# Performance work log

Hardware: AMD Instinct MI355X
Metric: run time of the kernel (lower is better)

The kernel has to match this reference:

```python
import jax, jax.numpy as jnp
import numpy as np

N = 50000       # num nodes
E = 800000      # num edges (before self loops)
D_IN = 128
D_H = 128
D_OUT = 40


def setup_inputs() -> dict:
    key = jax.random.key(0)
    ks = jax.random.split(key, 8)
    x = jax.random.normal(ks[0], (N, D_IN), dtype=jnp.float32)
    edge_index = jax.random.randint(ks[1], (2, E), 0, N, dtype=jnp.int32)
    # GCNConv weights (glorot-ish scale) and biases
    W1 = jax.random.normal(ks[2], (D_IN, D_H), dtype=jnp.float32) / np.sqrt(D_IN)
    b1 = jnp.zeros((D_H,), dtype=jnp.float32)
    W2 = jax.random.normal(ks[3], (D_H, D_H), dtype=jnp.float32) / np.sqrt(D_H)
    b2 = jnp.zeros((D_H,), dtype=jnp.float32)
    Wc = jax.random.normal(ks[4], (D_H, D_OUT), dtype=jnp.float32) / np.sqrt(D_H)
    bc = jnp.zeros((D_OUT,), dtype=jnp.float32)
    return {"x": x, "edge_index": edge_index, "W1": W1, "b1": b1,
            "W2": W2, "b2": b2, "Wc": Wc, "bc": bc}


def _gcn_conv(x, row, col, num_nodes, W, b):
    # PyG GCNConv: h = X @ W; out[c] += norm(r,c) * h[r]; out += b
    h = x @ W
    deg = jax.ops.segment_sum(jnp.ones(row.shape[0], h.dtype), col,
                              num_segments=num_nodes)
    dinv = jnp.where(deg > 0, jax.lax.rsqrt(deg), 0.0).astype(h.dtype)
    norm = dinv[row] * dinv[col]                      # [E+N]
    msg = h[row] * norm[:, None]                      # gather + scale
    agg = jax.ops.segment_sum(msg, col, num_segments=num_nodes)  # scatter-add
    return agg + b


def reference(x, edge_index, W1, b1, W2, b2, Wc, bc):
    # add self loops (GCNConv default add_self_loops=True)
    loops = jnp.arange(N, dtype=edge_index.dtype)
    row = jnp.concatenate([edge_index[0], loops])
    col = jnp.concatenate([edge_index[1], loops])
    h = jax.nn.relu(_gcn_conv(x, row, col, N, W1, b1))
    h = jax.nn.relu(_gcn_conv(h, row, col, N, W2, b2))
    g = jnp.mean(h, axis=0)                           # mean pool over nodes
    return g @ Wc + bc                                # [D_OUT]
```

## Files before the change

### kernel.cpp

```cpp
#include <hip/hip_runtime.h>
#include <hip/hip_fp16.h>


typedef _Float16 half8 __attribute__((ext_vector_type(8)));
typedef float f32x4 __attribute__((ext_vector_type(4)));
typedef float f32x2 __attribute__((ext_vector_type(2)));

constexpr int N = 50000;
constexpr int E = 800000;
constexpr int D = 128;
constexpr int DOUT = 40;
constexpr int CAP = 64;
constexpr int HB = 128;
constexpr int EPB = E / HB;
constexpr int HWRD = 12500;
constexpr int GM = (N + 127) / 128;
constexpr int NW = N / 4;
constexpr int GF = 3 * GM;
constexpr int GB2 = (N + 31) / 32;

__global__ __launch_bounds__(1024) void k_hist(const int* __restrict__ col,
                                               unsigned char* __restrict__ hist,
                                               unsigned char* __restrict__ rank,
                                               const float* __restrict__ W1,
                                               const float* __restrict__ W2,
                                               __half* __restrict__ T1,
                                               __half* __restrict__ T2) {
    __shared__ unsigned int h[HWRD];
    int b = blockIdx.x, t = threadIdx.x;
    if (b >= HB) {
        int o = (b - HB) * 1024 + t;
        const float* W = (o < 16384) ? W1 : W2;
        __half* T = (o < 16384) ? T1 : T2;
        int oo = o & 16383;
        int n = oo >> 7, k = oo & 127;
        T[oo] = (__half)W[k * 128 + n];
        return;
    }
    for (int i = t; i < HWRD; i += 1024) h[i] = 0;
    __syncthreads();
    int e0 = b * EPB;
    for (int e = e0 + t; e < e0 + EPB; e += 1024) {
        int c = col[e];
        unsigned int old = atomicAdd(&h[c >> 2], 1u << ((c & 3) * 8));
        rank[e] = (unsigned char)((old >> ((c & 3) * 8)) & 0xff);
    }
    __syncthreads();
    unsigned int* out = (unsigned int*)(hist + (size_t)b * 50000);
    for (int i = t; i < HWRD; i += 1024) out[i] = h[i];
}

__global__ void k_colscan(unsigned char* __restrict__ hist, int* __restrict__ deg,
                          float* __restrict__ dinv) {
    int c4 = blockIdx.x * 256 + threadIdx.x;
    if (c4 >= HWRD) return;
    unsigned int* hw = (unsigned int*)hist;
    unsigned int run = 0;
#pragma unroll 8
    for (int b = 0; b < HB; ++b) {
        unsigned int v = hw[b * HWRD + c4];
        hw[b * HWRD + c4] = run;
        run += v;
    }
#pragma unroll
    for (int j = 0; j < 4; ++j) {
        int dg = (run >> (8 * j)) & 0xff;
        deg[4 * c4 + j] = dg;
        dinv[4 * c4 + j] = rsqrtf((float)(dg + 1));
    }
}

__device__ __forceinline__ unsigned char f8enc(float v) {
    return (unsigned char)(__builtin_amdgcn_cvt_pk_fp8_f32(v, v, 0, false) & 0xff);
}
__device__ __forceinline__ void add8f8(float* a, uint2 u) {
    f32x2 f0 = __builtin_amdgcn_cvt_pk_f32_fp8(u.x, false);
    f32x2 f1 = __builtin_amdgcn_cvt_pk_f32_fp8(u.x, true);
    f32x2 f2 = __builtin_amdgcn_cvt_pk_f32_fp8(u.y, false);
    f32x2 f3 = __builtin_amdgcn_cvt_pk_f32_fp8(u.y, true);
    a[0] += f0[0]; a[1] += f0[1]; a[2] += f1[0]; a[3] += f1[1];
    a[4] += f2[0]; a[5] += f2[1]; a[6] += f3[0]; a[7] += f3[1];
}

__device__ __forceinline__ half8 ldA(const float* rowp, int koff) {
    float4 u0 = *(const float4*)(rowp + koff);
    float4 u1 = *(const float4*)(rowp + koff + 4);
    half8 r;
    r[0] = (_Float16)u0.x; r[1] = (_Float16)u0.y;
    r[2] = (_Float16)u0.z; r[3] = (_Float16)u0.w;
    r[4] = (_Float16)u1.x; r[5] = (_Float16)u1.y;
    r[6] = (_Float16)u1.z; r[7] = (_Float16)u1.w;
    return r;
}

__device__ __forceinline__ void mfma_gemm(const float* __restrict__ A,
                                          const __half* __restrict__ Wt,
                                          const float* __restrict__ dinv,
                                          unsigned char* __restrict__ out8,
                                          int row0, int tid) {
    int wave = tid >> 6, lane = tid & 63;
    int quad = lane >> 4, c16 = lane & 15;
    int m0 = row0 + wave * 32;
    int ra = m0 + c16;      if (ra >= N) ra = 0;
    int rb = m0 + 16 + c16; if (rb >= N) rb = 0;
    const float* pa = A + (size_t)ra * D;
    const float* pb = A + (size_t)rb * D;

    f32x4 acc[2][8];
#pragma unroll
    for (int i = 0; i < 2; ++i)
#pragma unroll
        for (int j = 0; j < 8; ++j) acc[i][j] = (f32x4){0.f, 0.f, 0.f, 0.f};

#pragma unroll
    for (int kq = 0; kq < 4; ++kq) {
        int koff = kq * 32 + quad * 8;
        half8 a0 = ldA(pa, koff);
        half8 a1 = ldA(pb, koff);
#pragma unroll
        for (int nt = 0; nt < 8; ++nt) {
            half8 bf = *(const half8*)(Wt + (size_t)(nt * 16 + c16) * D + koff);
            acc[0][nt] = __builtin_amdgcn_mfma_f32_16x16x32_f16(a0, bf, acc[0][nt], 0, 0, 0);
            acc[1][nt] = __builtin_amdgcn_mfma_f32_16x16x32_f16(a1, bf, acc[1][nt], 0, 0, 0);
        }
    }

#pragma unroll
    for (int rt = 0; rt < 2; ++rt) {
        int mt = m0 + rt * 16;
#pragma unroll
        for (int i = 0; i < 4; ++i) {
            int grow = mt + quad * 4 + i;
            if (grow < N) {
                float s = dinv[grow];
                unsigned char* orow = out8 + (size_t)grow * D + c16;
#pragma unroll
                for (int nt = 0; nt < 8; ++nt)
                    orow[nt * 16] = f8enc(acc[rt][nt][i] * s);
            }
        }
    }
}

__global__ __launch_bounds__(256) void k_fuse(const int* __restrict__ ei,
                                              const unsigned char* __restrict__ hist,
                                              const unsigned char* __restrict__ rank,
                                              unsigned short* __restrict__ csr,
                                              const float* __restrict__ x,
                                              const __half* __restrict__ Wt1,
                                              const float* __restrict__ dinv,
                                              unsigned char* __restrict__ out8) {
    int b = blockIdx.x, m = b % 3;
    if (m < 2) {
        int sb = (b / 3) * 2 + m;
        int e0 = sb * 1024 + threadIdx.x * 4;
        if (e0 >= E) return;
        int4 rr = *(const int4*)(ei + e0);
        int4 cc = *(const int4*)(ei + E + e0);
        uchar4 kk = *(const uchar4*)(rank + e0);
        int rs[4] = {rr.x, rr.y, rr.z, rr.w};
        int cs[4] = {cc.x, cc.y, cc.z, cc.w};
        int ks[4] = {kk.x, kk.y, kk.z, kk.w};
#pragma unroll
        for (int i = 0; i < 4; ++i) {
            int e = e0 + i;
            int c = cs[i];
            int chunk = e / EPB;
            int slot = (int)hist[(size_t)chunk * 50000 + c] + ks[i];
            if (slot < CAP) csr[(c << 6) + slot] = (unsigned short)rs[i];
        }
        return;
    }
    mfma_gemm(x, Wt1, dinv, out8, (b / 3) * 128, threadIdx.x);
}

__device__ __forceinline__ float agg_core(int c, int lane,
                                          const unsigned char* __restrict__ hs8,
                                          const int* __restrict__ deg,
                                          const unsigned short* __restrict__ csr,
                                          float* a0) {
    int qw = lane >> 4;
    int q  = lane & 15;
    int dgRaw = deg[c];
    int dg = dgRaw < CAP ? dgRaw : CAP;
    float dc = rsqrtf((float)(dgRaw + 1));
    int e0 = c << 6;

    float a1[8] = {0, 0, 0, 0, 0, 0, 0, 0};
    float a2[8] = {0, 0, 0, 0, 0, 0, 0, 0};
    float a3[8] = {0, 0, 0, 0, 0, 0, 0, 0};
#pragma unroll
    for (int t = 0; t < 8; ++t) a0[t] = 0.f;
    if (qw == 0)
        add8f8(a0, *(const uint2*)&hs8[(size_t)c * D + q * 8]);

    int j = 0;
    for (; j + 16 <= dg; j += 16) {
        int r0 = csr[e0 + j + qw];
        int r1 = csr[e0 + j + 4 + qw];
        int r2 = csr[e0 + j + 8 + qw];
        int r3 = csr[e0 + j + 12 + qw];
        uint2 u0 = *(const uint2*)&hs8[(size_t)r0 * D + q * 8];
        uint2 u1 = *(const uint2*)&hs8[(size_t)r1 * D + q * 8];
        uint2 u2 = *(const uint2*)&hs8[(size_t)r2 * D + q * 8];
        uint2 u3 = *(const uint2*)&hs8[(size_t)r3 * D + q * 8];
        add8f8(a0, u0); add8f8(a1, u1); add8f8(a2, u2); add8f8(a3, u3);
    }
    if (j + 8 <= dg) {
        int r0 = csr[e0 + j + qw];
        int r1 = csr[e0 + j + 4 + qw];
        uint2 u0 = *(const uint2*)&hs8[(size_t)r0 * D + q * 8];
        uint2 u1 = *(const uint2*)&hs8[(size_t)r1 * D + q * 8];
        add8f8(a0, u0); add8f8(a1, u1);
        j += 8;
    }
    if (j + 4 <= dg) {
        int r0 = csr[e0 + j + qw];
        add8f8(a0, *(const uint2*)&hs8[(size_t)r0 * D + q * 8]);
        j += 4;
    }
    int rem = dg - j;
    if (qw < rem) {
        int r0 = csr[e0 + j + qw];
        add8f8(a1, *(const uint2*)&hs8[(size_t)r0 * D + q * 8]);
    }

#pragma unroll
    for (int t = 0; t < 8; ++t) a0[t] += a1[t];
#pragma unroll
    for (int t = 0; t < 8; ++t) a2[t] += a3[t];
#pragma unroll
    for (int t = 0; t < 8; ++t) a0[t] += a2[t];
#pragma unroll
    for (int t = 0; t < 8; ++t) a0[t] += __shfl_xor(a0[t], 16, 64);
#pragma unroll
    for (int t = 0; t < 8; ++t) a0[t] += __shfl_xor(a0[t], 32, 64);
    return dc;
}

__global__ __launch_bounds__(512) void k_agg1g(const unsigned char* __restrict__ hs8,
                                               const int* __restrict__ deg,
                                               const unsigned short* __restrict__ csr,
                                               const float* __restrict__ bias,
                                               const __half* __restrict__ Wt2,
                                               const float* __restrict__ dinv,
                                               unsigned char* __restrict__ out8) {
    __shared__ __align__(16) __half As[32][136];
    int wave = threadIdx.x >> 6, lane = threadIdx.x & 63;
    int n0 = blockIdx.x * 32;
    int q = lane & 15;
#pragma unroll 1
    for (int i = 0; i < 4; ++i) {
        int c = n0 + wave * 4 + i;
        if (c < N) {
            float a0[8];
            float dc = agg_core(c, lane, hs8, deg, csr, a0);
            if ((lane >> 4) == 0) {
                union { __half2 h[4]; uint4 u; } p;
#pragma unroll
                for (int j2 = 0; j2 < 4; ++j2) {
                    float xv = fmaxf(fmaf(dc, a0[2 * j2],     bias[q * 8 + 2 * j2]),     0.f);
                    float yv = fmaxf(fmaf(dc, a0[2 * j2 + 1], bias[q * 8 + 2 * j2 + 1]), 0.f);
                    p.h[j2] = __floats2half2_rn(xv, yv);
                }
                *(uint4*)&As[wave * 4 + i][q * 8] = p.u;
            }
        } else if ((lane >> 4) == 0) {
            uint4 z = {0, 0, 0, 0};
            *(uint4*)&As[wave * 4 + i][q * 8] = z;
        }
    }
    __syncthreads();
    int quad = lane >> 4, c16 = lane & 15;
    f32x4 acc0 = (f32x4){0.f, 0.f, 0.f, 0.f};
    f32x4 acc1 = (f32x4){0.f, 0.f, 0.f, 0.f};
    const __half* bcol = Wt2 + (size_t)(wave * 16 + c16) * D;
#pragma unroll
    for (int kq = 0; kq < 4; ++kq) {
        int koff = kq * 32 + quad * 8;
        half8 a0 = *(const half8*)&As[c16][koff];
        half8 a1 = *(const half8*)&As[16 + c16][koff];
        half8 bf = *(const half8*)(bcol + koff);
        acc0 = __builtin_amdgcn_mfma_f32_16x16x32_f16(a0, bf, acc0, 0, 0, 0);
        acc1 = __builtin_amdgcn_mfma_f32_16x16x32_f16(a1, bf, acc1, 0, 0, 0);
    }
#pragma unroll
    for (int i = 0; i < 4; ++i) {
        int g0 = n0 + quad * 4 + i;
        if (g0 < N)
            out8[(size_t)g0 * D + wave * 16 + c16] = f8enc(acc0[i] * dinv[g0]);
        int g1 = n0 + 16 + quad * 4 + i;
        if (g1 < N)
            out8[(size_t)g1 * D + wave * 16 + c16] = f8enc(acc1[i] * dinv[g1]);
    }
}

__global__ __launch_bounds__(256) void k_agg2(const unsigned char* __restrict__ hs8,
                                              const int* __restrict__ deg,
                                              const unsigned short* __restrict__ csr,
                                              const float* __restrict__ bias,
                                              float* __restrict__ gpart) {
    __shared__ float gblk[4][128];
    int wave = threadIdx.x >> 6;
    int lane = threadIdx.x & 63;
    int c = blockIdx.x * 4 + wave;
    float a0[8];
    float dc = agg_core(c, lane, hs8, deg, csr, a0);
    if ((lane >> 4) == 0) {
        int q = lane & 15;
#pragma unroll
        for (int i = 0; i < 8; ++i)
            gblk[wave][q * 8 + i] = fmaxf(fmaf(dc, a0[i], bias[q * 8 + i]), 0.f);
    }
    __syncthreads();
    int t = threadIdx.x;
    if (t < 128)
        gpart[(size_t)blockIdx.x * 128 + t] =
            gblk[0][t] + gblk[1][t] + gblk[2][t] + gblk[3][t];
}

__global__ __launch_bounds__(256) void k_pool(const float* __restrict__ gpart,
                                              float* __restrict__ gpart2) {
    int d = threadIdx.x & 127;
    int half = threadIdx.x >> 7;
    int b = blockIdx.x;
    int per = (NW + 255) / 256;
    int r0 = b * per;
    int r1 = r0 + per;
    if (r1 > NW) r1 = NW;
    float acc = 0.f;
    for (int r = r0 + half; r < r1; r += 2)
        acc += gpart[(size_t)r * D + d];
    __shared__ float red[256];
    red[threadIdx.x] = acc;
    __syncthreads();
    if (half == 0) gpart2[(size_t)b * D + d] = red[d] + red[128 + d];
}

__global__ __launch_bounds__(512) void k_final(const float* __restrict__ gpart2,
                                               const float* __restrict__ Wc,
                                               const float* __restrict__ bc,
                                               float* __restrict__ out) {
    __shared__ float g[D];
    __shared__ float red[512];
    int t = threadIdx.x;
    int d = t & 127, grp = t >> 7;
    float s = 0.f;
#pragma unroll 4
    for (int w = grp * 64; w < grp * 64 + 64; ++w)
        s += gpart2[(size_t)w * D + d];
    red[t] = s;
    __syncthreads();
    if (grp == 0)
        g[d] = (red[d] + red[128 + d] + red[256 + d] + red[384 + d]) * (1.0f / (float)N);
    __syncthreads();
    if (t < DOUT) {
        float acc = bc[t];
        for (int dd = 0; dd < D; ++dd) acc = fmaf(g[dd], Wc[dd * DOUT + t], acc);
        out[t] = acc;
    }
}

extern "C" void kernel_launch(void* const* d_in, const int* in_sizes, int n_in,
                              void* d_out, int out_size, void* d_ws, size_t ws_size,
                              hipStream_t stream) {
    const float* x  = (const float*)d_in[0];
    const int*   ei = (const int*)d_in[1];
    const float* W1 = (const float*)d_in[2];
    const float* b1 = (const float*)d_in[3];
    const float* W2 = (const float*)d_in[4];
    const float* b2 = (const float*)d_in[5];
    const float* Wc = (const float*)d_in[6];
    const float* bc = (const float*)d_in[7];
    float* out = (float*)d_out;

    char* ws = (char*)d_ws;
    size_t off = 0;
    auto alloc = [&](size_t bytes) {
        void* p = ws + off;
        off += (bytes + 511) & ~(size_t)511;
        return p;
    };
    unsigned char*  hist   = (unsigned char*) alloc((size_t)HB * 50000);
    unsigned char*  rank   = (unsigned char*) alloc((size_t)E);
    int*            deg    = (int*)           alloc((size_t)N * 4);
    float*          dinv   = (float*)         alloc((size_t)N * 4);
    unsigned short* csr    = (unsigned short*)alloc((size_t)N * CAP * 2);
    unsigned char*  hs8    = (unsigned char*) alloc((size_t)N * D);
    unsigned char*  hs8b   = (unsigned char*) alloc((size_t)N * D);
    __half*         Wt1    = (__half*)        alloc((size_t)D * D * 2);
    __half*         Wt2    = (__half*)        alloc((size_t)D * D * 2);
    float*          gpart  = (float*)         alloc((size_t)NW * D * 4);
    float*          gpart2 = (float*)         alloc((size_t)256 * D * 4);
    (void)ws_size; (void)in_sizes; (void)n_in; (void)out_size;

    const int* col = ei + E;

    k_hist<<<HB + 32, 1024, 0, stream>>>(col, hist, rank, W1, W2, Wt1, Wt2);
    k_colscan<<<(HWRD + 255) / 256, 256, 0, stream>>>(hist, deg, dinv);
    k_fuse<<<GF, 256, 0, stream>>>(ei, hist, rank, csr, x, Wt1, dinv, hs8);
    k_agg1g<<<GB2, 512, 0, stream>>>(hs8, deg, csr, b1, Wt2, dinv, hs8b);
    k_agg2<<<NW, 256, 0, stream>>>(hs8b, deg, csr, b2, gpart);
    k_pool<<<256, 256, 0, stream>>>(gpart, gpart2);
    k_final<<<1, 512, 0, stream>>>(gpart2, Wc, bc, out);
}
```

Before: 213.6 us.

## Give each wave one node in the layer-1 aggregation-GEMM kernel

Previously each 512-thread block handled 32 nodes, with every wave aggregating 4 nodes one after another before a shared 32-row MFMA GEMM. Now each 256-thread block handles 4 nodes, one per wave, launched with N/4 blocks. Each wave then computes two 16-column output tiles. This removes the serial per-wave aggregation loop and exposes more concurrent gather latency. In exchange, each MFMA uses only 4 of its 16 rows (the rest of the shared tile is never written), and Wt2 is re-read per block across many more blocks.

Result: slower. 229.9 us (+7.7%).

```diff
diff --git a/kernel.cpp b/kernel.cpp
--- a/kernel.cpp
+++ b/kernel.cpp
@@ -17,7 +17,6 @@
 constexpr int GM = (N + 127) / 128;
 constexpr int NW = N / 4;
 constexpr int GF = 3 * GM;
-constexpr int GB2 = (N + 31) / 32;
 
 __global__ __launch_bounds__(1024) void k_hist(const int* __restrict__ col,
                                                unsigned char* __restrict__ hist,
@@ -238,60 +237,51 @@
     return dc;
 }
 
-__global__ __launch_bounds__(512) void k_agg1g(const unsigned char* __restrict__ hs8,
+__global__ __launch_bounds__(256) void k_agg1g(const unsigned char* __restrict__ hs8,
                                                const int* __restrict__ deg,
                                                const unsigned short* __restrict__ csr,
                                                const float* __restrict__ bias,
                                                const __half* __restrict__ Wt2,
                                                const float* __restrict__ dinv,
                                                unsigned char* __restrict__ out8) {
-    __shared__ __align__(16) __half As[32][136];
+    __shared__ __align__(16) __half As[16][136];
     int wave = threadIdx.x >> 6, lane = threadIdx.x & 63;
-    int n0 = blockIdx.x * 32;
+    int c = blockIdx.x * 4 + wave;
+    float a0[8];
+    float dc = agg_core(c, lane, hs8, deg, csr, a0);
     int q = lane & 15;
-#pragma unroll 1
-    for (int i = 0; i < 4; ++i) {
-        int c = n0 + wave * 4 + i;
-        if (c < N) {
-            float a0[8];
-            float dc = agg_core(c, lane, hs8, deg, csr, a0);
-            if ((lane >> 4) == 0) {
-                union { __half2 h[4]; uint4 u; } p;
-#pragma unroll
-                for (int j2 = 0; j2 < 4; ++j2) {
-                    float xv = fmaxf(fmaf(dc, a0[2 * j2],     bias[q * 8 + 2 * j2]),     0.f);
-                    float yv = fmaxf(fmaf(dc, a0[2 * j2 + 1], bias[q * 8 + 2 * j2 + 1]), 0.f);
-                    p.h[j2] = __floats2half2_rn(xv, yv);
-                }
-                *(uint4*)&As[wave * 4 + i][q * 8] = p.u;
+    if ((lane >> 4) == 0) {
+        union { __half2 h[4]; uint4 u; } p;
+#pragma unroll
+        for (int j2 = 0; j2 < 4; ++j2) {
+            float xv = fmaxf(fmaf(dc, a0[2 * j2],     bias[q * 8 + 2 * j2]),     0.f);
+            float yv = fmaxf(fmaf(dc, a0[2 * j2 + 1], bias[q * 8 + 2 * j2 + 1]), 0.f);
+            p.h[j2] = __floats2half2_rn(xv, yv);
+        }
+        *(uint4*)&As[wave][q * 8] = p.u;
+    }
+    __syncthreads();
+    int quad = lane >> 4, c16 = lane & 15;
+    int n0 = blockIdx.x * 4;
+#pragma unroll
+    for (int t = 0; t < 2; ++t) {
+        int nt = wave * 2 + t;
+        f32x4 acc = (f32x4){0.f, 0.f, 0.f, 0.f};
+        const __half* bcol = Wt2 + (size_t)(nt * 16 + c16) * D;
+#pragma unroll
+        for (int kq = 0; kq < 4; ++kq) {
+            int koff = kq * 32 + quad * 8;
+            half8 av = *(const half8*)&As[c16][koff];
+            half8 bv = *(const half8*)(bcol + koff);
+            acc = __builtin_amdgcn_mfma_f32_16x16x32_f16(av, bv, acc, 0, 0, 0);
+        }
+        if (quad == 0) {
+#pragma unroll
+            for (int i = 0; i < 4; ++i) {
+                int node = n0 + i;
+                out8[(size_t)node * D + nt * 16 + c16] = f8enc(acc[i] * dinv[node]);
             }
-        } else if ((lane >> 4) == 0) {
-            uint4 z = {0, 0, 0, 0};
-            *(uint4*)&As[wave * 4 + i][q * 8] = z;
-        }
-    }
-    __syncthreads();
-    int quad = lane >> 4, c16 = lane & 15;
-    f32x4 acc0 = (f32x4){0.f, 0.f, 0.f, 0.f};
-    f32x4 acc1 = (f32x4){0.f, 0.f, 0.f, 0.f};
-    const __half* bcol = Wt2 + (size_t)(wave * 16 + c16) * D;
-#pragma unroll
-    for (int kq = 0; kq < 4; ++kq) {
-        int koff = kq * 32 + quad * 8;
-        half8 a0 = *(const half8*)&As[c16][koff];
-        half8 a1 = *(const half8*)&As[16 + c16][koff];
-        half8 bf = *(const half8*)(bcol + koff);
-        acc0 = __builtin_amdgcn_mfma_f32_16x16x32_f16(a0, bf, acc0, 0, 0, 0);
-        acc1 = __builtin_amdgcn_mfma_f32_16x16x32_f16(a1, bf, acc1, 0, 0, 0);
-    }
-#pragma unroll
-    for (int i = 0; i < 4; ++i) {
-        int g0 = n0 + quad * 4 + i;
-        if (g0 < N)
-            out8[(size_t)g0 * D + wave * 16 + c16] = f8enc(acc0[i] * dinv[g0]);
-        int g1 = n0 + 16 + quad * 4 + i;
-        if (g1 < N)
-            out8[(size_t)g1 * D + wave * 16 + c16] = f8enc(acc1[i] * dinv[g1]);
+        }
     }
 }
 
@@ -399,7 +389,7 @@
     k_hist<<<HB + 32, 1024, 0, stream>>>(col, hist, rank, W1, W2, Wt1, Wt2);
     k_colscan<<<(HWRD + 255) / 256, 256, 0, stream>>>(hist, deg, dinv);
     k_fuse<<<GF, 256, 0, stream>>>(ei, hist, rank, csr, x, Wt1, dinv, hs8);
-    k_agg1g<<<GB2, 512, 0, stream>>>(hs8, deg, csr, b1, Wt2, dinv, hs8b);
+    k_agg1g<<<NW, 256, 0, stream>>>(hs8, deg, csr, b1, Wt2, dinv, hs8b);
     k_agg2<<<NW, 256, 0, stream>>>(hs8b, deg, csr, b2, gpart);
     k_pool<<<256, 256, 0, stream>>>(gpart, gpart2);
     k_final<<<1, 512, 0, stream>>>(gpart2, Wc, bc, out);
```
